# Performance work log

Hardware: AMD Instinct MI355X
Metric: run time of the kernel (lower is better)

## Reference

```python
import jax, jax.numpy as jnp
import numpy as np

B, A, C, G = 16, 65472, 81, 50
POS_THRESH = 0.5        # positive_threshold
NEG_POS_RATIO = 3
CENTER_VAR, SIZE_VAR = 0.1, 0.2   # standard SSD encoding variances
BETA = 1.0 / 9


def _make_boxes(key, shape):
    # random valid corner-form boxes in [0,1]
    k1, k2 = jax.random.split(key)
    cxy = jax.random.uniform(k1, shape + (2,), minval=0.1, maxval=0.9)
    wh = jax.random.uniform(k2, shape + (2,), minval=0.05, maxval=0.3)
    lo = jnp.clip(cxy - wh / 2, 0.0, 1.0)
    hi = jnp.clip(cxy + wh / 2, 0.0, 1.0)
    return jnp.concatenate([lo, hi], axis=-1).astype(jnp.float32)


def setup_inputs() -> dict:
    key = jax.random.key(0)
    ks = jax.random.split(key, 6)
    confidence = jax.random.normal(ks[0], (B, A, C), dtype=jnp.float32)
    predicted_locations = jax.random.normal(ks[1], (B, A, 4), dtype=jnp.float32)
    boxes = _make_boxes(ks[2], (B, G))
    labels = jax.random.randint(ks[3], (B, G, 1), 1, C).astype(jnp.float32)
    gts = jnp.concatenate([boxes, labels], axis=-1)          # (B, G, 5)
    counts = jax.random.randint(ks[4], (B,), 1, G + 1)       # valid gt per image
    anchors = _make_boxes(ks[5], (A,))                        # corner form
    return {"confidence": confidence, "predicted_locations": predicted_locations,
            "gts": gts, "counts": counts, "anchors": anchors}


def _center_form(b):
    # corner (x1,y1,x2,y2) -> center (cx,cy,w,h)
    return jnp.concatenate([(b[..., :2] + b[..., 2:]) * 0.5,
                            b[..., 2:] - b[..., :2]], axis=-1)


def _iou(a, b):
    # a: (A,4), b: (G,4), corner form -> (A,G)
    lt = jnp.maximum(a[:, None, :2], b[None, :, :2])
    rb = jnp.minimum(a[:, None, 2:], b[None, :, 2:])
    wh = jnp.clip(rb - lt, 0.0)
    inter = wh[..., 0] * wh[..., 1]
    area_a = (a[:, 2] - a[:, 0]) * (a[:, 3] - a[:, 1])
    area_b = (b[:, 2] - b[:, 0]) * (b[:, 3] - b[:, 1])
    return inter / (area_a[:, None] + area_b[None, :] - inter + 1e-10)


def _encode(matched, anchors_c):
    m = _center_form(matched)
    g_cxcy = (m[..., :2] - anchors_c[..., :2]) / (anchors_c[..., 2:] * CENTER_VAR)
    g_wh = jnp.log(m[..., 2:] / anchors_c[..., 2:] + 1e-10) / SIZE_VAR
    return jnp.concatenate([g_cxcy, g_wh], axis=-1)


def _match(gt, count, anchors, anchors_c):
    # gt: (G,5), count: scalar int
    boxes = gt[:, :4]
    glabels = gt[:, 4].astype(jnp.int32)
    valid = jnp.arange(boxes.shape[0]) < count
    ious = jnp.where(valid[None, :], _iou(anchors, boxes), -1.0)  # (A,G)
    best_iou = ious.max(axis=1)          # best gt per anchor
    best_idx = ious.argmax(axis=1)
    best_anchor = ious.argmax(axis=0)    # best anchor per gt (G,)
    # force-match: each valid gt claims its best anchor (invalid -> dropped)
    scat = jnp.where(valid, best_anchor, anchors.shape[0])
    best_idx = best_idx.at[scat].set(jnp.arange(boxes.shape[0]), mode='drop')
    best_iou = best_iou.at[scat].set(2.0, mode='drop')
    labels = jnp.where(best_iou < POS_THRESH, 0, glabels[best_idx])  # (A,)
    loc = _encode(boxes[best_idx], anchors_c)                         # (A,4)
    return labels, loc


def reference(confidence, predicted_locations, gts, counts, anchors):
    anchors_c = _center_form(anchors)
    labels, gt_locations = jax.vmap(
        lambda g, c: _match(g, c, anchors, anchors_c))(gts, counts)
    labels = jax.lax.stop_gradient(labels)
    gt_locations = jax.lax.stop_gradient(gt_locations)

    logp = jax.nn.log_softmax(confidence, axis=2)          # (B,A,C)
    pos_mask = labels > 0
    num_pos_b = pos_mask.sum(axis=1)                        # (B,)

    # hard negative mining on background loss (positives excluded via -inf)
    mining = jnp.where(pos_mask, -jnp.inf, jax.lax.stop_gradient(-logp[:, :, 0]))
    order = jnp.argsort(-mining, axis=1)   # descending
    rank = jnp.argsort(order, axis=1)
    neg_mask = rank < (NEG_POS_RATIO * num_pos_b)[:, None]
    mask = pos_mask | neg_mask

    num_pos = jnp.maximum(1.0, pos_mask.sum().astype(jnp.float32))

    # masked cross-entropy (sum) == F.cross_entropy(conf[mask], labels[mask], 'sum')
    ce = -jnp.take_along_axis(logp, labels[..., None], axis=2)[..., 0]
    classification_loss = jnp.sum(jnp.where(mask, ce, 0.0)) / (num_pos * 4.0)

    # smooth L1 over positive anchors only
    n = jnp.abs(predicted_locations - gt_locations)
    sl1 = jnp.where(n < BETA, 0.5 * n * n / BETA, n - 0.5 * BETA)
    localisation_loss = jnp.sum(jnp.where(pos_mask[..., None], sl1, 0.0)) / (num_pos * 4.0)
    return (localisation_loss, classification_loss)
```

## Files before the change

kernel.cpp:

```cpp
#include <hip/hip_runtime.h>
#include <math.h>

#define Bn 16
#define An 65472
#define Cn 81
#define Gn 50
#define ROWS 128
#define NBUCK 1024
#define LISTCAP 8192

static_assert((Bn * (long long)An) % ROWS == 0, "rows divide");

constexpr float POS_THRESH_C = 0.5f;
constexpr float BETA_C = 1.0f / 9.0f;

typedef const __attribute__((address_space(1))) void GPTR;
typedef __attribute__((address_space(3))) void LPTR;

__global__ __launch_bounds__(64) void k0_zero(int* __restrict__ numpos_b,
                                              float* __restrict__ fsums) {
    int t = threadIdx.x;
    if (t < Bn) numpos_b[t] = 0;
    if (t == 32) fsums[0] = 0.f;
    if (t == 33) fsums[1] = 0.f;
}

__global__ __launch_bounds__(256) void k0b_zero(int* __restrict__ ghist) {
    ghist[blockIdx.x * 256 + threadIdx.x] = 0;
}

__global__ __launch_bounds__(256) void k1a(const float* __restrict__ anchors,
                                           const float* __restrict__ gts,
                                           const int* __restrict__ counts,
                                           float* __restrict__ best_iou,
                                           int* __restrict__ best_idx) {
    const int b = blockIdx.y;
    __shared__ float sg[Gn * 5];
    const int t = threadIdx.x;
    if (t < Gn * 5) sg[t] = gts[b * Gn * 5 + t];
    __syncthreads();
    const int a = blockIdx.x * 256 + t;
    if (a >= An) return;
    const int cnt = counts[b];
    const float4 av = ((const float4*)anchors)[a];
    const float area_a = (av.z - av.x) * (av.w - av.y);
    float best = -1.0f;
    int bidx = 0;
    for (int g = 0; g < Gn; ++g) {
        if (g >= cnt) break;
        const float bx0 = sg[g * 5 + 0], by0 = sg[g * 5 + 1];
        const float bx1 = sg[g * 5 + 2], by1 = sg[g * 5 + 3];
        const float w = fmaxf(fminf(av.z, bx1) - fmaxf(av.x, bx0), 0.f);
        const float h = fmaxf(fminf(av.w, by1) - fmaxf(av.y, by0), 0.f);
        const float inter = w * h;
        const float area_b = (bx1 - bx0) * (by1 - by0);
        const float iou = inter / (area_a + area_b - inter + 1e-10f);
        if (iou > best) { best = iou; bidx = g; }
    }
    best_iou[(size_t)b * An + a] = best;
    best_idx[(size_t)b * An + a] = bidx;
}

__global__ __launch_bounds__(256) void k1b(const float* __restrict__ anchors,
                                           const float* __restrict__ gts,
                                           const int* __restrict__ counts,
                                           int* __restrict__ best_anchor) {
    const int b = blockIdx.y, g = blockIdx.x;
    const int t = threadIdx.x;
    const int cnt = counts[b];
    if (g >= cnt) { if (t == 0) best_anchor[b * Gn + g] = 0; return; }
    const float bx0 = gts[(b * Gn + g) * 5 + 0], by0 = gts[(b * Gn + g) * 5 + 1];
    const float bx1 = gts[(b * Gn + g) * 5 + 2], by1 = gts[(b * Gn + g) * 5 + 3];
    const float area_b = (bx1 - bx0) * (by1 - by0);
    const float4* a4 = (const float4*)anchors;
    float best = -2.f;
    int bidx = 0x7fffffff;
    for (int base = t; base < An; base += 1024) {
        const int a1 = base + 256, a2 = base + 512, a3 = base + 768;
        const float4 av0 = a4[base];
        float4 av1, av2, av3;
        const bool ok1 = a1 < An, ok2 = a2 < An, ok3 = a3 < An;
        if (ok1) av1 = a4[a1];
        if (ok2) av2 = a4[a2];
        if (ok3) av3 = a4[a3];
        {
            const float area_a = (av0.z - av0.x) * (av0.w - av0.y);
            const float w = fmaxf(fminf(av0.z, bx1) - fmaxf(av0.x, bx0), 0.f);
            const float h = fmaxf(fminf(av0.w, by1) - fmaxf(av0.y, by0), 0.f);
            const float inter = w * h;
            const float iou = inter / (area_a + area_b - inter + 1e-10f);
            if (iou > best) { best = iou; bidx = base; }
        }
        if (ok1) {
            const float area_a = (av1.z - av1.x) * (av1.w - av1.y);
            const float w = fmaxf(fminf(av1.z, bx1) - fmaxf(av1.x, bx0), 0.f);
            const float h = fmaxf(fminf(av1.w, by1) - fmaxf(av1.y, by0), 0.f);
            const float inter = w * h;
            const float iou = inter / (area_a + area_b - inter + 1e-10f);
            if (iou > best) { best = iou; bidx = a1; }
        }
        if (ok2) {
            const float area_a = (av2.z - av2.x) * (av2.w - av2.y);
            const float w = fmaxf(fminf(av2.z, bx1) - fmaxf(av2.x, bx0), 0.f);
            const float h = fmaxf(fminf(av2.w, by1) - fmaxf(av2.y, by0), 0.f);
            const float inter = w * h;
            const float iou = inter / (area_a + area_b - inter + 1e-10f);
            if (iou > best) { best = iou; bidx = a2; }
        }
        if (ok3) {
            const float area_a = (av3.z - av3.x) * (av3.w - av3.y);
            const float w = fmaxf(fminf(av3.z, bx1) - fmaxf(av3.x, bx0), 0.f);
            const float h = fmaxf(fminf(av3.w, by1) - fmaxf(av3.y, by0), 0.f);
            const float inter = w * h;
            const float iou = inter / (area_a + area_b - inter + 1e-10f);
            if (iou > best) { best = iou; bidx = a3; }
        }
    }
    __shared__ float rv[256];
    __shared__ int ri[256];
    rv[t] = best; ri[t] = bidx;
    __syncthreads();
    for (int s = 128; s > 0; s >>= 1) {
        if (t < s) {
            const float fv = rv[t + s]; const int fi = ri[t + s];
            if (fv > rv[t] || (fv == rv[t] && fi < ri[t])) { rv[t] = fv; ri[t] = fi; }
        }
        __syncthreads();
    }
    if (t == 0) best_anchor[b * Gn + g] = ri[0];
}

__global__ __launch_bounds__(64) void k1c(const int* __restrict__ counts,
                                          const int* __restrict__ best_anchor,
                                          float* __restrict__ best_iou,
                                          int* __restrict__ best_idx) {
    const int b = threadIdx.x;
    if (b >= Bn) return;
    const int cnt = counts[b] < Gn ? counts[b] : Gn;
    for (int g = 0; g < cnt; ++g) {
        const int a = best_anchor[b * Gn + g];
        best_idx[(size_t)b * An + a] = g;
        best_iou[(size_t)b * An + a] = 2.0f;
    }
}

__global__ __launch_bounds__(256) void k2(const float* __restrict__ conf,
                                          const float* __restrict__ pred,
                                          const float* __restrict__ gts,
                                          const float* __restrict__ anchors,
                                          const float* __restrict__ best_iou,
                                          const int* __restrict__ best_idx,
                                          int* __restrict__ v_int,
                                          int* __restrict__ numpos_b,
                                          float* __restrict__ fsums) {
    __shared__ __align__(16) float sc[ROWS * Cn];
    __shared__ float s_ce[4], s_loc[4];
    __shared__ int s_n0[4], s_n1[4];
    const int t = threadIdx.x;
    {
        const float* gp = conf + (size_t)blockIdx.x * (ROWS * Cn);
#pragma unroll
        for (int k = 0; k < 10; ++k) {
            const int c = k * 256 + t;
            __builtin_amdgcn_global_load_lds((GPTR*)(gp + c * 4), (LPTR*)(sc + c * 4), 16, 0, 0);
        }
        if (t < 32) {
            const int c = 2560 + t;
            __builtin_amdgcn_global_load_lds((GPTR*)(gp + c * 4), (LPTR*)(sc + c * 4), 16, 0, 0);
        }
    }
    __syncthreads();
    const int r = t >> 1, h = t & 1;
    const float* row = sc + r * Cn;
    const int j0 = h ? 41 : 0;
    const int j1 = h ? Cn : 41;
    float s0 = 0.f, s1 = 0.f;
    for (int j = j0; j + 1 < j1; j += 2) { s0 += __expf(row[j]); s1 += __expf(row[j + 1]); }
    if (((j1 - j0) & 1) != 0) s0 += __expf(row[j1 - 1]);
    const float s = s0 + s1;
    const float S = s + __shfl_xor(s, 1);
    const float lse = logf(S);

    float ce = 0.f, loc = 0.f;
    int n0 = 0, n1 = 0;
    const int bf = (int)(((size_t)blockIdx.x * ROWS) / An);
    if (h == 0) {
        const size_t gidx = (size_t)blockIdx.x * ROWS + r;
        const int b = (int)(gidx / An);
        const int a = (int)(gidx - (size_t)b * An);
        const float bi = best_iou[gidx];
        const int idx = best_idx[gidx];
        if (bi < POS_THRESH_C) {
            v_int[gidx] = __float_as_int(lse - row[0]);
        } else {
            v_int[gidx] = -1;
            int lab = (int)gts[((size_t)b * Gn + idx) * 5 + 4];
            lab = lab < 0 ? 0 : (lab > Cn - 1 ? Cn - 1 : lab);
            ce = lse - row[lab];
            if (b == bf) n0 = 1; else n1 = 1;
            const float bx0 = gts[((size_t)b * Gn + idx) * 5 + 0];
            const float by0 = gts[((size_t)b * Gn + idx) * 5 + 1];
            const float bx1 = gts[((size_t)b * Gn + idx) * 5 + 2];
            const float by1 = gts[((size_t)b * Gn + idx) * 5 + 3];
            const float4 av = ((const float4*)anchors)[a];
            const float acx = (av.x + av.z) * 0.5f, acy = (av.y + av.w) * 0.5f;
            const float aw = av.z - av.x, ah = av.w - av.y;
            float tt[4];
            tt[0] = ((bx0 + bx1) * 0.5f - acx) / (aw * 0.1f);
            tt[1] = ((by0 + by1) * 0.5f - acy) / (ah * 0.1f);
            tt[2] = logf((bx1 - bx0) / aw + 1e-10f) / 0.2f;
            tt[3] = logf((by1 - by0) / ah + 1e-10f) / 0.2f;
            const float4 p = ((const float4*)pred)[gidx];
            const float pk[4] = {p.x, p.y, p.z, p.w};
#pragma unroll
            for (int k = 0; k < 4; ++k) {
                const float n = fabsf(pk[k] - tt[k]);
                loc += (n < BETA_C) ? 0.5f * n * n / BETA_C : n - 0.5f * BETA_C;
            }
        }
    }
#pragma unroll
    for (int off = 32; off > 0; off >>= 1) {
        ce += __shfl_down(ce, off);
        loc += __shfl_down(loc, off);
        n0 += __shfl_down(n0, off);
        n1 += __shfl_down(n1, off);
    }
    if ((t & 63) == 0) {
        const int w = t >> 6;
        s_ce[w] = ce; s_loc[w] = loc; s_n0[w] = n0; s_n1[w] = n1;
    }
    __syncthreads();
    if (t == 0) {
        const float CE = s_ce[0] + s_ce[1] + s_ce[2] + s_ce[3];
        const float LC = s_loc[0] + s_loc[1] + s_loc[2] + s_loc[3];
        const int N0 = s_n0[0] + s_n0[1] + s_n0[2] + s_n0[3];
        const int N1 = s_n1[0] + s_n1[1] + s_n1[2] + s_n1[3];
        if (CE != 0.f) atomicAdd(&fsums[0], CE);
        if (LC != 0.f) atomicAdd(&fsums[1], LC);
        if (N0 > 0) atomicAdd(&numpos_b[bf], N0);
        if (N1 > 0) atomicAdd(&numpos_b[bf + 1], N1);
    }
}

__global__ __launch_bounds__(256) void k3a(const int* __restrict__ v_int,
                                           int* __restrict__ ghist) {
    const int b = blockIdx.y, c = blockIdx.x;
    __shared__ int lh[NBUCK];
    const int t = threadIdx.x;
    for (int i = t; i < NBUCK; i += 256) lh[i] = 0;
    __syncthreads();
    const int4* v4 = (const int4*)(v_int + (size_t)b * An) + c * 1023;
    for (int i = t; i < 1023; i += 256) {
        const int4 x4 = v4[i];
        const int xs[4] = {x4.x, x4.y, x4.z, x4.w};
#pragma unroll
        for (int q = 0; q < 4; ++q) {
            const int x = xs[q];
            if (x < 0) continue;
            int bin = (int)(__int_as_float(x) * 64.0f);
            bin = bin > NBUCK - 1 ? NBUCK - 1 : bin;
            atomicAdd(&lh[bin], 1);
        }
    }
    __syncthreads();
    for (int i = t; i < NBUCK; i += 256) {
        const int cv = lh[i];
        if (cv) atomicAdd(&ghist[b * NBUCK + i], cv);
    }
}

__global__ __launch_bounds__(256) void k3b(const int* __restrict__ v_int,
                                           const int* __restrict__ ghist,
                                           const int* __restrict__ numpos_b,
                                           float* __restrict__ neg_sum_b) {
    const int b = blockIdx.x, t = threadIdx.x;
    const int npb = numpos_b[b];
    const long long K = 3LL * npb;
    const int n_nonpos = An - npb;
    __shared__ int h[NBUCK];
    __shared__ int gsfx[256];
    __shared__ int s_kt, s_r, s_m;
    __shared__ float fred[256];
    __shared__ float list[LISTCAP];
    if (K <= 0) { if (t == 0) neg_sum_b[b] = 0.f; return; }
    const int4* v4 = (const int4*)(v_int + (size_t)b * An);
    const int N4 = An / 4;
    const bool selAll = (K >= n_nonpos);
    int kt = -1, r = 0;
    if (!selAll) {
        for (int i = t; i < NBUCK; i += 256) h[i] = ghist[b * NBUCK + i];
        if (t == 0) s_m = 0;
        __syncthreads();
        gsfx[t] = h[4 * t] + h[4 * t + 1] + h[4 * t + 2] + h[4 * t + 3];
        __syncthreads();
        if (t == 0) {
            int acc = 0;
            for (int i = 255; i >= 0; --i) { const int tmp = gsfx[i]; gsfx[i] = acc; acc += tmp; }
        }
        __syncthreads();
        {
            const int base = 4 * t;
            int cg[4];
            cg[3] = gsfx[t];
            cg[2] = cg[3] + h[base + 3];
            cg[1] = cg[2] + h[base + 2];
            cg[0] = cg[1] + h[base + 1];
#pragma unroll
            for (int q = 0; q < 4; ++q) {
                if (cg[q] < K && K <= cg[q] + (long long)h[base + q]) {
                    s_kt = base + q; s_r = (int)(K - cg[q]);
                }
            }
        }
        __syncthreads();
        kt = s_kt; r = s_r;
    } else {
        if (t == 0) s_m = 0;
        __syncthreads();
    }
    float s = 0.f;
    for (int i = t; i < N4; i += 256) {
        const int4 x4 = v4[i];
        const int xs[4] = {x4.x, x4.y, x4.z, x4.w};
#pragma unroll
        for (int q = 0; q < 4; ++q) {
            const int x = xs[q];
            if (x < 0) continue;
            const float v = __int_as_float(x);
            if (selAll) { s += v; continue; }
            int bin = (int)(v * 64.0f);
            bin = bin > NBUCK - 1 ? NBUCK - 1 : bin;
            if (bin > kt) s += v;
            else if (bin == kt) {
                const int p = atomicAdd(&s_m, 1);
                if (p < LISTCAP) list[p] = v;
            }
        }
    }
    __syncthreads();
    if (!selAll) {
        int M = s_m; M = M > LISTCAP ? LISTCAP : M;
        for (int i = t; i < M; i += 256) {
            const float x = list[i];
            int cnt = 0;
            for (int j = 0; j < M; ++j) {
                const float y = list[j];
                cnt += (y > x) || (y == x && j < i);
            }
            if (cnt < r) s += x;
        }
    }
    fred[t] = s;
    __syncthreads();
    for (int st = 128; st > 0; st >>= 1) {
        if (t < st) fred[t] += fred[t + st];
        __syncthreads();
    }
    if (t == 0) neg_sum_b[b] = fred[0];
}

__global__ __launch_bounds__(64) void k4(const int* __restrict__ numpos_b,
                                         const float* __restrict__ fsums,
                                         const float* __restrict__ neg_sum_b,
                                         float* __restrict__ out) {
    if (threadIdx.x == 0) {
        int np = 0;
        for (int b = 0; b < Bn; ++b) np += numpos_b[b];
        const float num_pos = fmaxf(1.f, (float)np);
        const float denom = num_pos * 4.f;
        float neg = 0.f;
        for (int b = 0; b < Bn; ++b) neg += neg_sum_b[b];
        out[0] = fsums[1] / denom;
        out[1] = (fsums[0] + neg) / denom;
    }
}

extern "C" void kernel_launch(void* const* d_in, const int* in_sizes, int n_in,
                              void* d_out, int out_size, void* d_ws, size_t ws_size,
                              hipStream_t stream) {
    const float* conf    = (const float*)d_in[0];
    const float* pred    = (const float*)d_in[1];
    const float* gts     = (const float*)d_in[2];
    const int*   counts  = (const int*)d_in[3];
    const float* anchors = (const float*)d_in[4];
    float* out = (float*)d_out;

    const size_t BA = (size_t)Bn * An;
    char* w = (char*)d_ws;
    float* best_iou    = (float*)w; w += BA * sizeof(float);
    int*   best_idx    = (int*)w;   w += BA * sizeof(int);
    int*   v_int       = (int*)w;   w += BA * sizeof(int);
    int*   best_anchor = (int*)w;   w += Bn * Gn * sizeof(int);
    int*   numpos_b    = (int*)w;   w += 64;
    float* fsums       = (float*)w; w += 64;
    float* neg_sum_b   = (float*)w; w += 64;
    int*   ghist       = (int*)best_iou;

    hipLaunchKernelGGL(k0_zero, dim3(1), dim3(64), 0, stream, numpos_b, fsums);
    hipLaunchKernelGGL(k1a, dim3((An + 255) / 256, Bn), dim3(256), 0, stream,
                       anchors, gts, counts, best_iou, best_idx);
    hipLaunchKernelGGL(k1b, dim3(Gn, Bn), dim3(256), 0, stream,
                       anchors, gts, counts, best_anchor);
    hipLaunchKernelGGL(k1c, dim3(1), dim3(64), 0, stream,
                       counts, best_anchor, best_iou, best_idx);
    hipLaunchKernelGGL(k2, dim3((unsigned)(BA / ROWS)), dim3(256), 0, stream,
                       conf, pred, gts, anchors, best_iou, best_idx,
                       v_int, numpos_b, fsums);
    hipLaunchKernelGGL(k0b_zero, dim3(Bn * NBUCK / 256), dim3(256), 0, stream, ghist);
    hipLaunchKernelGGL(k3a, dim3(16, Bn), dim3(256), 0, stream, v_int, ghist);
    hipLaunchKernelGGL(k3b, dim3(Bn), dim3(256), 0, stream,
                       v_int, ghist, numpos_b, neg_sum_b);
    hipLaunchKernelGGL(k4, dim3(1), dim3(64), 0, stream, numpos_b, fsums, neg_sum_b, out);
}
```

Measured before the change: 750.3 us.

## Fuse histogram build into softmax kernel and halve rows per block

The histogram pass (k3a) is folded into k2: each non-positive anchor's background loss is binned and atomically added straight to the global histogram, which removes a separate read of v_int and one kernel launch. ROWS drops to 64 and each row is now split across four threads, with a launch-bounds occupancy hint added. Blocks now never straddle batches, so the per-block positive count is simpler. The two zeroing kernels are merged, and ghist moves to its own workspace region so it can be zeroed before k2. The trade-off is many global atomics on a few hot bins in place of LDS-privatised counts, which may contend.

```diff
diff --git a/kernel.cpp b/kernel.cpp
--- a/kernel.cpp
+++ b/kernel.cpp
@@ -5,11 +5,11 @@
 #define An 65472
 #define Cn 81
 #define Gn 50
-#define ROWS 128
+#define ROWS 64
 #define NBUCK 1024
 #define LISTCAP 8192
 
-static_assert((Bn * (long long)An) % ROWS == 0, "rows divide");
+static_assert((An % ROWS) == 0, "blocks never straddle batches");
 
 constexpr float POS_THRESH_C = 0.5f;
 constexpr float BETA_C = 1.0f / 9.0f;
@@ -17,16 +17,16 @@
 typedef const __attribute__((address_space(1))) void GPTR;
 typedef __attribute__((address_space(3))) void LPTR;
 
-__global__ __launch_bounds__(64) void k0_zero(int* __restrict__ numpos_b,
-                                              float* __restrict__ fsums) {
-    int t = threadIdx.x;
-    if (t < Bn) numpos_b[t] = 0;
-    if (t == 32) fsums[0] = 0.f;
-    if (t == 33) fsums[1] = 0.f;
-}
-
-__global__ __launch_bounds__(256) void k0b_zero(int* __restrict__ ghist) {
-    ghist[blockIdx.x * 256 + threadIdx.x] = 0;
+__global__ __launch_bounds__(256) void k0_zero(int* __restrict__ numpos_b,
+                                               float* __restrict__ fsums,
+                                               int* __restrict__ ghist) {
+    const int t = threadIdx.x;
+    if (blockIdx.x == 64) {
+        if (t < Bn) numpos_b[t] = 0;
+        if (t == 32) { fsums[0] = 0.f; fsums[1] = 0.f; }
+    } else {
+        ghist[blockIdx.x * 256 + t] = 0;
+    }
 }
 
 __global__ __launch_bounds__(256) void k1a(const float* __restrict__ anchors,
@@ -144,60 +144,65 @@
     }
 }
 
-__global__ __launch_bounds__(256) void k2(const float* __restrict__ conf,
-                                          const float* __restrict__ pred,
-                                          const float* __restrict__ gts,
-                                          const float* __restrict__ anchors,
-                                          const float* __restrict__ best_iou,
-                                          const int* __restrict__ best_idx,
-                                          int* __restrict__ v_int,
-                                          int* __restrict__ numpos_b,
-                                          float* __restrict__ fsums) {
+__global__ __launch_bounds__(256, 7) void k2(const float* __restrict__ conf,
+                                             const float* __restrict__ pred,
+                                             const float* __restrict__ gts,
+                                             const float* __restrict__ anchors,
+                                             const float* __restrict__ best_iou,
+                                             const int* __restrict__ best_idx,
+                                             int* __restrict__ v_int,
+                                             int* __restrict__ numpos_b,
+                                             float* __restrict__ fsums,
+                                             int* __restrict__ ghist) {
     __shared__ __align__(16) float sc[ROWS * Cn];
     __shared__ float s_ce[4], s_loc[4];
-    __shared__ int s_n0[4], s_n1[4];
+    __shared__ int s_n[4];
     const int t = threadIdx.x;
     {
         const float* gp = conf + (size_t)blockIdx.x * (ROWS * Cn);
 #pragma unroll
-        for (int k = 0; k < 10; ++k) {
+        for (int k = 0; k < 5; ++k) {
             const int c = k * 256 + t;
             __builtin_amdgcn_global_load_lds((GPTR*)(gp + c * 4), (LPTR*)(sc + c * 4), 16, 0, 0);
         }
-        if (t < 32) {
-            const int c = 2560 + t;
+        if (t < 16) {
+            const int c = 1280 + t;
             __builtin_amdgcn_global_load_lds((GPTR*)(gp + c * 4), (LPTR*)(sc + c * 4), 16, 0, 0);
         }
     }
     __syncthreads();
-    const int r = t >> 1, h = t & 1;
+    const int r = t >> 2, h = t & 3;
     const float* row = sc + r * Cn;
-    const int j0 = h ? 41 : 0;
-    const int j1 = h ? Cn : 41;
+    const int j0 = h * 20 + (h != 0);
+    const int j1 = 21 + h * 20;
     float s0 = 0.f, s1 = 0.f;
     for (int j = j0; j + 1 < j1; j += 2) { s0 += __expf(row[j]); s1 += __expf(row[j + 1]); }
     if (((j1 - j0) & 1) != 0) s0 += __expf(row[j1 - 1]);
-    const float s = s0 + s1;
-    const float S = s + __shfl_xor(s, 1);
-    const float lse = logf(S);
+    float s = s0 + s1;
+    s += __shfl_xor(s, 1);
+    s += __shfl_xor(s, 2);
+    const float lse = logf(s);
 
     float ce = 0.f, loc = 0.f;
-    int n0 = 0, n1 = 0;
-    const int bf = (int)(((size_t)blockIdx.x * ROWS) / An);
+    int n = 0;
+    const int b = blockIdx.x / (An / ROWS);
     if (h == 0) {
         const size_t gidx = (size_t)blockIdx.x * ROWS + r;
-        const int b = (int)(gidx / An);
         const int a = (int)(gidx - (size_t)b * An);
         const float bi = best_iou[gidx];
         const int idx = best_idx[gidx];
         if (bi < POS_THRESH_C) {
-            v_int[gidx] = __float_as_int(lse - row[0]);
+            const float v = lse - row[0];
+            v_int[gidx] = __float_as_int(v);
+            int bin = (int)(v * 64.0f);
+            bin = bin < 0 ? 0 : (bin > NBUCK - 1 ? NBUCK - 1 : bin);
+            atomicAdd(&ghist[b * NBUCK + bin], 1);
         } else {
             v_int[gidx] = -1;
             int lab = (int)gts[((size_t)b * Gn + idx) * 5 + 4];
             lab = lab < 0 ? 0 : (lab > Cn - 1 ? Cn - 1 : lab);
             ce = lse - row[lab];
-            if (b == bf) n0 = 1; else n1 = 1;
+            n = 1;
             const float bx0 = gts[((size_t)b * Gn + idx) * 5 + 0];
             const float by0 = gts[((size_t)b * Gn + idx) * 5 + 1];
             const float bx1 = gts[((size_t)b * Gn + idx) * 5 + 2];
@@ -214,8 +219,8 @@
             const float pk[4] = {p.x, p.y, p.z, p.w};
 #pragma unroll
             for (int k = 0; k < 4; ++k) {
-                const float n = fabsf(pk[k] - tt[k]);
-                loc += (n < BETA_C) ? 0.5f * n * n / BETA_C : n - 0.5f * BETA_C;
+                const float nn = fabsf(pk[k] - tt[k]);
+                loc += (nn < BETA_C) ? 0.5f * nn * nn / BETA_C : nn - 0.5f * BETA_C;
             }
         }
     }
@@ -223,50 +228,20 @@
     for (int off = 32; off > 0; off >>= 1) {
         ce += __shfl_down(ce, off);
         loc += __shfl_down(loc, off);
-        n0 += __shfl_down(n0, off);
-        n1 += __shfl_down(n1, off);
+        n += __shfl_down(n, off);
     }
     if ((t & 63) == 0) {
         const int w = t >> 6;
-        s_ce[w] = ce; s_loc[w] = loc; s_n0[w] = n0; s_n1[w] = n1;
+        s_ce[w] = ce; s_loc[w] = loc; s_n[w] = n;
     }
     __syncthreads();
     if (t == 0) {
         const float CE = s_ce[0] + s_ce[1] + s_ce[2] + s_ce[3];
         const float LC = s_loc[0] + s_loc[1] + s_loc[2] + s_loc[3];
-        const int N0 = s_n0[0] + s_n0[1] + s_n0[2] + s_n0[3];
-        const int N1 = s_n1[0] + s_n1[1] + s_n1[2] + s_n1[3];
+        const int N = s_n[0] + s_n[1] + s_n[2] + s_n[3];
         if (CE != 0.f) atomicAdd(&fsums[0], CE);
         if (LC != 0.f) atomicAdd(&fsums[1], LC);
-        if (N0 > 0) atomicAdd(&numpos_b[bf], N0);
-        if (N1 > 0) atomicAdd(&numpos_b[bf + 1], N1);
-    }
-}
-
-__global__ __launch_bounds__(256) void k3a(const int* __restrict__ v_int,
-                                           int* __restrict__ ghist) {
-    const int b = blockIdx.y, c = blockIdx.x;
-    __shared__ int lh[NBUCK];
-    const int t = threadIdx.x;
-    for (int i = t; i < NBUCK; i += 256) lh[i] = 0;
-    __syncthreads();
-    const int4* v4 = (const int4*)(v_int + (size_t)b * An) + c * 1023;
-    for (int i = t; i < 1023; i += 256) {
-        const int4 x4 = v4[i];
-        const int xs[4] = {x4.x, x4.y, x4.z, x4.w};
-#pragma unroll
-        for (int q = 0; q < 4; ++q) {
-            const int x = xs[q];
-            if (x < 0) continue;
-            int bin = (int)(__int_as_float(x) * 64.0f);
-            bin = bin > NBUCK - 1 ? NBUCK - 1 : bin;
-            atomicAdd(&lh[bin], 1);
-        }
-    }
-    __syncthreads();
-    for (int i = t; i < NBUCK; i += 256) {
-        const int cv = lh[i];
-        if (cv) atomicAdd(&ghist[b * NBUCK + i], cv);
+        if (N > 0) atomicAdd(&numpos_b[b], N);
     }
 }
 
@@ -395,9 +370,9 @@
     int*   numpos_b    = (int*)w;   w += 64;
     float* fsums       = (float*)w; w += 64;
     float* neg_sum_b   = (float*)w; w += 64;
-    int*   ghist       = (int*)best_iou;
-
-    hipLaunchKernelGGL(k0_zero, dim3(1), dim3(64), 0, stream, numpos_b, fsums);
+    int*   ghist       = (int*)w;   w += Bn * NBUCK * sizeof(int);
+
+    hipLaunchKernelGGL(k0_zero, dim3(65), dim3(256), 0, stream, numpos_b, fsums, ghist);
     hipLaunchKernelGGL(k1a, dim3((An + 255) / 256, Bn), dim3(256), 0, stream,
                        anchors, gts, counts, best_iou, best_idx);
     hipLaunchKernelGGL(k1b, dim3(Gn, Bn), dim3(256), 0, stream,
@@ -406,9 +381,7 @@
                        counts, best_anchor, best_iou, best_idx);
     hipLaunchKernelGGL(k2, dim3((unsigned)(BA / ROWS)), dim3(256), 0, stream,
                        conf, pred, gts, anchors, best_iou, best_idx,
-                       v_int, numpos_b, fsums);
-    hipLaunchKernelGGL(k0b_zero, dim3(Bn * NBUCK / 256), dim3(256), 0, stream, ghist);
-    hipLaunchKernelGGL(k3a, dim3(16, Bn), dim3(256), 0, stream, v_int, ghist);
+                       v_int, numpos_b, fsums, ghist);
     hipLaunchKernelGGL(k3b, dim3(Bn), dim3(256), 0, stream,
                        v_int, ghist, numpos_b, neg_sum_b);
     hipLaunchKernelGGL(k4, dim3(1), dim3(64), 0, stream, numpos_b, fsums, neg_sum_b, out);
```

New measurement: 980.9 us. 30.7% more time.
